# Optimization experiments

Measured on AMD Instinct MI355X. Metric: run time of the kernel, lower is better.

## Reference

```python
import jax, jax.numpy as jnp
import numpy as np

N, F_IN, F_OUT, HEADS = 4096, 128, 64, 4


def setup_inputs() -> dict:
    key = jax.random.key(0)
    k1, k2, k3, k4, k5 = jax.random.split(key, 5)
    X = jax.random.normal(k1, (N, F_IN), dtype=jnp.float32)
    A = jax.random.randint(k2, (N, N), 0, 2, dtype=jnp.int32)
    # zero the diagonal: the torch loop always prepends the self node, so the
    # adjacency must not also contain it (would duplicate the self term).
    A = A * (1 - jnp.eye(N, dtype=jnp.int32))
    # per-head Linear(F_IN, F_OUT) weights/bias and Linear(2*F_OUT, 1, bias=False)
    W = jax.random.normal(k3, (HEADS, F_OUT, F_IN), dtype=jnp.float32) / np.sqrt(F_IN)
    b = jax.random.normal(k4, (HEADS, F_OUT), dtype=jnp.float32) * 0.02
    att = jax.random.normal(k5, (HEADS, 2 * F_OUT), dtype=jnp.float32) / np.sqrt(2 * F_OUT)
    return {"X": X, "A": A, "W": W, "b": b, "att": att}


def reference(X, A, W, b, att):
    # H[h, n, o] = line_h(X)
    H = jnp.einsum('nf,hof->hno', X, W) + b[:, None, :]
    f_out = W.shape[1]
    a_src, a_dst = att[:, :f_out], att[:, f_out:]
    # score e_ij = leaky_relu(a_src.H_i + a_dst.H_j)
    s = jnp.einsum('hno,ho->hn', H, a_src)  # query-side term (xi_bar expanded)
    d = jnp.einsum('hno,ho->hn', H, a_dst)  # neighbor-side term
    e = jax.nn.leaky_relu(s[:, :, None] + d[:, None, :])  # [H, N, N]
    # neighbor set = {self} U {j : A_ij != 0}
    mask = (A > 0) | jnp.eye(A.shape[0], dtype=bool)
    e = jnp.where(mask[None], e, -jnp.inf)
    alpha = jax.nn.softmax(e, axis=-1)  # segment softmax per node row
    # weighted sum per head, then mean over heads (sum / head in the original)
    out = jnp.einsum('hnm,hmo->no', alpha, H) / W.shape[0]
    return out  # [N, F_OUT]
```

## Files before the change

### kernel.cpp

```cpp
#include <hip/hip_runtime.h>
#include <hip/hip_bf16.h>


#define NN 4096
#define FIN 128
#define FOUT 64
#define NH 4

typedef __attribute__((ext_vector_type(8))) short bf16x8;
typedef __attribute__((ext_vector_type(4))) float f32x4;
typedef __attribute__((ext_vector_type(4))) unsigned int u32x4;

__device__ __forceinline__ unsigned short f32_bf16(float f) {
    unsigned u = __builtin_bit_cast(unsigned, f);
    u += 0x7fffu + ((u >> 16) & 1u);
    return (unsigned short)(u >> 16);
}
__device__ __forceinline__ float bf16_f32(unsigned short h) {
    unsigned u = ((unsigned)h) << 16;
    return __builtin_bit_cast(float, u);
}

__global__ __launch_bounds__(256) void pack_bits(
    const int* __restrict__ A, unsigned long long* __restrict__ Abits)
{
    const int row  = blockIdx.x;
    const int lane = threadIdx.x & 63;
    const int wv   = threadIdx.x >> 6;
    const int* arow = A + (size_t)row * NN;
    #pragma unroll 4
    for (int c = 0; c < 16; ++c) {
        const int col = c * 256 + wv * 64 + lane;
        unsigned long long m = __ballot(arow[col] > 0);
        if (lane == 0) Abits[(size_t)row * 64 + c * 4 + wv] = m;
    }
}

__global__ __launch_bounds__(256) void gat_prep(
    const float* __restrict__ X, const float* __restrict__ W,
    const float* __restrict__ b, const float* __restrict__ att,
    unsigned short* __restrict__ HbfT,
    float* __restrict__ s_out, float* __restrict__ d_out,
    float* __restrict__ es_g, float* __restrict__ es2_g,
    float* __restrict__ ed_g, float* __restrict__ ed2_g)
{
    const int rb = blockIdx.x;
    const int h  = blockIdx.y;
    const int n0 = rb * 32;
    const int t  = threadIdx.x;

    __shared__ float Xl[32][132];
    __shared__ float Wt[128][68];

    for (int g = t; g < 32 * 32; g += 256) {
        int row = g >> 5, c4 = g & 31;
        float4 v = *(const float4*)&X[(size_t)(n0 + row) * FIN + c4 * 4];
        *(float4*)&Xl[row][c4 * 4] = v;
    }
    for (int g = t; g < 64 * 32; g += 256) {
        int o = g >> 5, c4 = g & 31;
        float4 v = *(const float4*)&W[((size_t)h * FOUT + o) * FIN + c4 * 4];
        Wt[c4 * 4 + 0][o] = v.x; Wt[c4 * 4 + 1][o] = v.y;
        Wt[c4 * 4 + 2][o] = v.z; Wt[c4 * 4 + 3][o] = v.w;
    }
    __syncthreads();

    const int rg = t >> 4;
    const int og = t & 15;
    float acc[2][4] = {};

    #pragma unroll 4
    for (int f4 = 0; f4 < 32; ++f4) {
        float xv[2][4], wv[4][4];
        #pragma unroll
        for (int i = 0; i < 2; ++i) {
            float4 tmp = *(const float4*)&Xl[rg * 2 + i][f4 * 4];
            xv[i][0] = tmp.x; xv[i][1] = tmp.y; xv[i][2] = tmp.z; xv[i][3] = tmp.w;
        }
        #pragma unroll
        for (int k = 0; k < 4; ++k) {
            float4 tmp = *(const float4*)&Wt[f4 * 4 + k][og * 4];
            wv[k][0] = tmp.x; wv[k][1] = tmp.y; wv[k][2] = tmp.z; wv[k][3] = tmp.w;
        }
        #pragma unroll
        for (int i = 0; i < 2; ++i)
            #pragma unroll
            for (int k = 0; k < 4; ++k)
                #pragma unroll
                for (int jj = 0; jj < 4; ++jj)
                    acc[i][jj] = fmaf(xv[i][k], wv[k][jj], acc[i][jj]);
    }

    float bb[4], as_[4], ad_[4];
    #pragma unroll
    for (int jj = 0; jj < 4; ++jj) {
        bb[jj]  = b[h * FOUT + og * 4 + jj];
        as_[jj] = att[h * 2 * FOUT + og * 4 + jj];
        ad_[jj] = att[h * 2 * FOUT + FOUT + og * 4 + jj];
    }
    #pragma unroll
    for (int i = 0; i < 2; ++i)
        #pragma unroll
        for (int jj = 0; jj < 4; ++jj)
            acc[i][jj] += bb[jj];

    float sp[2] = {0.f, 0.f}, dp[2] = {0.f, 0.f};
    #pragma unroll
    for (int i = 0; i < 2; ++i)
        #pragma unroll
        for (int jj = 0; jj < 4; ++jj) {
            sp[i] = fmaf(acc[i][jj], as_[jj], sp[i]);
            dp[i] = fmaf(acc[i][jj], ad_[jj], dp[i]);
        }
    #pragma unroll
    for (int off = 1; off < 16; off <<= 1) {
        #pragma unroll
        for (int i = 0; i < 2; ++i) {
            sp[i] += __shfl_xor(sp[i], off);
            dp[i] += __shfl_xor(dp[i], off);
        }
    }
    if (og == 0) {
        #pragma unroll
        for (int i = 0; i < 2; ++i) {
            int nn = n0 + rg * 2 + i;
            s_out[h * NN + nn]  = sp[i];
            d_out[h * NN + nn]  = dp[i];
            es_g [h * NN + nn]  = __expf(sp[i]);
            es2_g[h * NN + nn]  = __expf(0.01f * sp[i]);
            ed_g [h * NN + nn]  = __expf(dp[i]);
            ed2_g[h * NN + nn]  = __expf(0.01f * dp[i]);
        }
    }

    #pragma unroll
    for (int jj = 0; jj < 4; ++jj) {
        int o = og * 4 + jj;
        ushort2 p;
        p.x = f32_bf16(acc[0][jj]);
        p.y = f32_bf16(acc[1][jj]);
        *(ushort2*)&HbfT[((size_t)h * FOUT + o) * NN + n0 + rg * 2] = p;
    }
}

__global__ __launch_bounds__(512, 8) void gat_main(
    const unsigned* __restrict__ Abits, const unsigned short* __restrict__ HbfT,
    const float* __restrict__ es_g, const float* __restrict__ es2_g,
    const float* __restrict__ ed_g, const float* __restrict__ ed2_g,
    float* __restrict__ Hpart, float* __restrict__ lpartP)
{
    const int n0 = blockIdx.x * 128;
    const int cg = blockIdx.y;
    const int h  = blockIdx.z;
    const int tid  = threadIdx.x;
    const int w    = tid >> 6;
    const int lane = tid & 63;
    const int r    = lane & 15;
    const int q    = lane >> 4;

    __shared__ unsigned short Hlds[64][256];
    __shared__ unsigned bits_lds[128 * 9];

    const int n  = n0 + w * 16 + r;
    const float es  = es_g [h * NN + n];
    const float es2 = es2_g[h * NN + n];
    const int bits_base = (w * 16 + r) * 9;
    const int qs = q * 8;

    bf16x8 ones;
    #pragma unroll
    for (int i = 0; i < 8; ++i) ones[i] = (short)0x3F80;

    f32x4 acc0 = {0,0,0,0}, acc1 = {0,0,0,0}, acc2 = {0,0,0,0},
          acc3 = {0,0,0,0}, accl = {0,0,0,0};

    for (int ch = 0; ch < 4; ++ch) {
        const int c0 = cg * 1024 + ch * 256;
        __syncthreads();

        #pragma unroll
        for (int it = 0; it < 4; ++it) {
            int flat = it * 512 + tid;
            int o    = flat >> 5;
            int c16  = flat & 31;
            int blk  = c16 ^ (o & 31);
            *(bf16x8*)&Hlds[o][blk * 8] =
                *(const bf16x8*)&HbfT[((size_t)h * FOUT + o) * NN + c0 + c16 * 8];
        }
        #pragma unroll
        for (int it = 0; it < 2; ++it) {
            int flat = it * 512 + tid;
            int row = flat >> 3, wd = flat & 7;
            bits_lds[row * 9 + wd] = Abits[(size_t)(n0 + row) * 128 + (c0 >> 5) + wd];
        }
        __syncthreads();

        const float* edh  = ed_g  + h * NN + c0;
        const float* ed2h = ed2_g + h * NN + c0;

        #pragma unroll
        for (int step = 0; step < 8; ++step) {
            const unsigned bits8 = bits_lds[bits_base + step] >> qs;
            const int mk = step * 32 + qs;

            const float4 e0 = *(const float4*)&edh [mk];
            const float4 e1 = *(const float4*)&edh [mk + 4];
            const float4 g0 = *(const float4*)&ed2h[mk];
            const float4 g1 = *(const float4*)&ed2h[mk + 4];
            const float edv [8] = {e0.x, e0.y, e0.z, e0.w, e1.x, e1.y, e1.z, e1.w};
            const float ed2v[8] = {g0.x, g0.y, g0.z, g0.w, g1.x, g1.y, g1.z, g1.w};

            u32x4 afu;
            #pragma unroll
            for (int p = 0; p < 4; ++p) {
                const int j0 = 2 * p, j1 = 2 * p + 1;
                float wa = (bits8 & (1u << j0))
                         ? fmaxf(es * edv[j0], es2 * ed2v[j0]) : 0.0f;
                float wb = (bits8 & (1u << j1))
                         ? fmaxf(es * edv[j1], es2 * ed2v[j1]) : 0.0f;
                __hip_bfloat162 pk = __float22bfloat162_rn(make_float2(wa, wb));
                unsigned u;
                __builtin_memcpy(&u, &pk, sizeof(u));
                afu[p] = u;
            }
            const bf16x8 af = __builtin_bit_cast(bf16x8, afu);

            const int mb = step * 4 + q;
            const bf16x8 b0 = *(const bf16x8*)&Hlds[r     ][(mb ^ ((r     ) & 31)) * 8];
            const bf16x8 b1 = *(const bf16x8*)&Hlds[r + 16][(mb ^ ((r + 16) & 31)) * 8];
            const bf16x8 b2 = *(const bf16x8*)&Hlds[r + 32][(mb ^ ((r + 32) & 31)) * 8];
            const bf16x8 b3 = *(const bf16x8*)&Hlds[r + 48][(mb ^ ((r + 48) & 31)) * 8];

            acc0 = __builtin_amdgcn_mfma_f32_16x16x32_bf16(af, b0,   acc0, 0, 0, 0);
            acc1 = __builtin_amdgcn_mfma_f32_16x16x32_bf16(af, b1,   acc1, 0, 0, 0);
            acc2 = __builtin_amdgcn_mfma_f32_16x16x32_bf16(af, b2,   acc2, 0, 0, 0);
            acc3 = __builtin_amdgcn_mfma_f32_16x16x32_bf16(af, b3,   acc3, 0, 0, 0);
            accl = __builtin_amdgcn_mfma_f32_16x16x32_bf16(af, ones, accl, 0, 0, 0);
        }
    }

    float* hb = Hpart + ((size_t)(cg * NH + h) * NN + n0 + w * 16) * FOUT;
    #pragma unroll
    for (int reg = 0; reg < 4; ++reg) {
        const int rr = q * 4 + reg;
        hb[rr * FOUT +  0 + r] = acc0[reg];
        hb[rr * FOUT + 16 + r] = acc1[reg];
        hb[rr * FOUT + 32 + r] = acc2[reg];
        hb[rr * FOUT + 48 + r] = acc3[reg];
    }
    if (r == 0) {
        #pragma unroll
        for (int reg = 0; reg < 4; ++reg)
            lpartP[(size_t)(cg * NH + h) * NN + n0 + w * 16 + q * 4 + reg] = accl[reg];
    }
}

__global__ __launch_bounds__(256) void gat_fin(
    const float* __restrict__ Hpart, const unsigned short* __restrict__ HbfT,
    const float* __restrict__ lpartP, const float* __restrict__ s_g,
    const float* __restrict__ d_g, float* __restrict__ out)
{
    const int tid = threadIdx.x;
    const int rr  = tid >> 4;
    const int c4  = tid & 15;
    const int n   = blockIdx.x * 16 + rr;
    const int o   = c4 * 4;

    float4 res = make_float4(0.f, 0.f, 0.f, 0.f);
    #pragma unroll
    for (int h = 0; h < NH; ++h) {
        float l = 0.f;
        #pragma unroll
        for (int cg = 0; cg < 4; ++cg)
            l += lpartP[(size_t)(cg * NH + h) * NN + n];
        float tt = s_g[h * NN + n] + d_g[h * NN + n];
        float wd = __expf(fmaxf(tt, 0.01f * tt));
        float inv = 0.25f / (l + wd);

        float4 ha = make_float4(0.f, 0.f, 0.f, 0.f);
        #pragma unroll
        for (int cg = 0; cg < 4; ++cg) {
            float4 hp = *(const float4*)&Hpart[((size_t)(cg * NH + h) * NN + n) * FOUT + o];
            ha.x += hp.x; ha.y += hp.y; ha.z += hp.z; ha.w += hp.w;
        }
        float hd[4];
        #pragma unroll
        for (int jj = 0; jj < 4; ++jj)
            hd[jj] = bf16_f32(HbfT[((size_t)h * FOUT + o + jj) * NN + n]);

        res.x += (ha.x + wd * hd[0]) * inv;
        res.y += (ha.y + wd * hd[1]) * inv;
        res.z += (ha.z + wd * hd[2]) * inv;
        res.w += (ha.w + wd * hd[3]) * inv;
    }
    *(float4*)&out[(size_t)n * FOUT + o] = res;
}

extern "C" void kernel_launch(void* const* d_in, const int* in_sizes, int n_in,
                              void* d_out, int out_size, void* d_ws, size_t ws_size,
                              hipStream_t stream) {
    const float* X   = (const float*)d_in[0];
    const int*   A   = (const int*)  d_in[1];
    const float* W   = (const float*)d_in[2];
    const float* b   = (const float*)d_in[3];
    const float* att = (const float*)d_in[4];
    float* out = (float*)d_out;

    char* ws = (char*)d_ws;
    unsigned short* HbfT = (unsigned short*)ws;
    size_t off = (size_t)NH * FOUT * NN * 2;
    float* s_buf   = (float*)(ws + off);  off += (size_t)NH * NN * 4;
    float* d_buf   = (float*)(ws + off);  off += (size_t)NH * NN * 4;
    float* es_buf  = (float*)(ws + off);  off += (size_t)NH * NN * 4;
    float* es2_buf = (float*)(ws + off);  off += (size_t)NH * NN * 4;
    float* ed_buf  = (float*)(ws + off);  off += (size_t)NH * NN * 4;
    float* ed2_buf = (float*)(ws + off);  off += (size_t)NH * NN * 4;
    unsigned long long* Abits = (unsigned long long*)(ws + off);
    off += (size_t)NN * 64 * 8;
    float* Hpart  = (float*)(ws + off);
    off += (size_t)4 * NH * NN * FOUT * 4;
    float* lpartP = (float*)(ws + off);
    off += (size_t)4 * NH * NN * 4;

    pack_bits<<<NN, 256, 0, stream>>>(A, Abits);
    gat_prep<<<dim3(128, 4), 256, 0, stream>>>(X, W, b, att, HbfT, s_buf, d_buf,
                                               es_buf, es2_buf, ed_buf, ed2_buf);
    gat_main<<<dim3(32, 4, 4), 512, 0, stream>>>((const unsigned*)Abits, HbfT,
                                                 es_buf, es2_buf, ed_buf, ed2_buf,
                                                 Hpart, lpartP);
    gat_fin<<<256, 256, 0, stream>>>(Hpart, HbfT, lpartP, s_buf, d_buf, out);
}
```

Baseline: 188.5 us.

## Retile GAT main kernel to 64-row blocks with 2-way column split and streaming hints

```diff
diff --git a/kernel.cpp b/kernel.cpp
--- a/kernel.cpp
+++ b/kernel.cpp
@@ -15,10 +15,6 @@
     unsigned u = __builtin_bit_cast(unsigned, f);
     u += 0x7fffu + ((u >> 16) & 1u);
     return (unsigned short)(u >> 16);
-}
-__device__ __forceinline__ float bf16_f32(unsigned short h) {
-    unsigned u = ((unsigned)h) << 16;
-    return __builtin_bit_cast(float, u);
 }
 
 __global__ __launch_bounds__(256) void pack_bits(
@@ -31,7 +27,7 @@
     #pragma unroll 4
     for (int c = 0; c < 16; ++c) {
         const int col = c * 256 + wv * 64 + lane;
-        unsigned long long m = __ballot(arow[col] > 0);
+        unsigned long long m = __ballot(__builtin_nontemporal_load(&arow[col]) > 0);
         if (lane == 0) Abits[(size_t)row * 64 + c * 4 + wv] = m;
     }
 }
@@ -39,7 +35,7 @@
 __global__ __launch_bounds__(256) void gat_prep(
     const float* __restrict__ X, const float* __restrict__ W,
     const float* __restrict__ b, const float* __restrict__ att,
-    unsigned short* __restrict__ HbfT,
+    unsigned short* __restrict__ HbfT, float* __restrict__ Hrow,
     float* __restrict__ s_out, float* __restrict__ d_out,
     float* __restrict__ es_g, float* __restrict__ es2_g,
     float* __restrict__ ed_g, float* __restrict__ ed2_g)
@@ -134,6 +130,11 @@
     }
 
     #pragma unroll
+    for (int i = 0; i < 2; ++i) {
+        float4 v = make_float4(acc[i][0], acc[i][1], acc[i][2], acc[i][3]);
+        *(float4*)&Hrow[((size_t)h * NN + n0 + rg * 2 + i) * FOUT + og * 4] = v;
+    }
+    #pragma unroll
     for (int jj = 0; jj < 4; ++jj) {
         int o = og * 4 + jj;
         ushort2 p;
@@ -143,29 +144,32 @@
     }
 }
 
-__global__ __launch_bounds__(512, 8) void gat_main(
+__global__ __launch_bounds__(256, 8) void gat_main(
     const unsigned* __restrict__ Abits, const unsigned short* __restrict__ HbfT,
     const float* __restrict__ es_g, const float* __restrict__ es2_g,
     const float* __restrict__ ed_g, const float* __restrict__ ed2_g,
     float* __restrict__ Hpart, float* __restrict__ lpartP)
 {
-    const int n0 = blockIdx.x * 128;
-    const int cg = blockIdx.y;
-    const int h  = blockIdx.z;
+    const int id  = blockIdx.x;
+    const int grp = id & 7;
+    const int h   = grp >> 1;
+    const int cg  = grp & 1;
+    const int bx  = id >> 3;
+    const int n0  = bx * 64;
     const int tid  = threadIdx.x;
     const int w    = tid >> 6;
     const int lane = tid & 63;
     const int r    = lane & 15;
     const int q    = lane >> 4;
-
-    __shared__ unsigned short Hlds[64][256];
-    __shared__ unsigned bits_lds[128 * 9];
-
-    const int n  = n0 + w * 16 + r;
+    const int qs   = q * 8;
+
+    __shared__ unsigned short Hlds[64][128];
+    __shared__ unsigned bits_lds[64 * 5];
+
+    const int n = n0 + w * 16 + r;
     const float es  = es_g [h * NN + n];
     const float es2 = es2_g[h * NN + n];
-    const int bits_base = (w * 16 + r) * 9;
-    const int qs = q * 8;
+    const int bits_base = (w * 16 + r) * 5;
 
     bf16x8 ones;
     #pragma unroll
@@ -174,24 +178,22 @@
     f32x4 acc0 = {0,0,0,0}, acc1 = {0,0,0,0}, acc2 = {0,0,0,0},
           acc3 = {0,0,0,0}, accl = {0,0,0,0};
 
-    for (int ch = 0; ch < 4; ++ch) {
-        const int c0 = cg * 1024 + ch * 256;
+    for (int ch = 0; ch < 16; ++ch) {
+        const int c0 = cg * 2048 + ch * 128;
         __syncthreads();
 
         #pragma unroll
         for (int it = 0; it < 4; ++it) {
-            int flat = it * 512 + tid;
-            int o    = flat >> 5;
-            int c16  = flat & 31;
-            int blk  = c16 ^ (o & 31);
+            int flat = it * 256 + tid;
+            int o    = flat >> 4;
+            int c16  = flat & 15;
+            int blk  = c16 ^ (o & 15);
             *(bf16x8*)&Hlds[o][blk * 8] =
                 *(const bf16x8*)&HbfT[((size_t)h * FOUT + o) * NN + c0 + c16 * 8];
         }
-        #pragma unroll
-        for (int it = 0; it < 2; ++it) {
-            int flat = it * 512 + tid;
-            int row = flat >> 3, wd = flat & 7;
-            bits_lds[row * 9 + wd] = Abits[(size_t)(n0 + row) * 128 + (c0 >> 5) + wd];
+        {
+            int row = tid >> 2, wd = tid & 3;
+            bits_lds[row * 5 + wd] = Abits[(size_t)(n0 + row) * 128 + (c0 >> 5) + wd];
         }
         __syncthreads();
 
@@ -199,7 +201,7 @@
         const float* ed2h = ed2_g + h * NN + c0;
 
         #pragma unroll
-        for (int step = 0; step < 8; ++step) {
+        for (int step = 0; step < 4; ++step) {
             const unsigned bits8 = bits_lds[bits_base + step] >> qs;
             const int mk = step * 32 + qs;
 
@@ -225,11 +227,11 @@
             }
             const bf16x8 af = __builtin_bit_cast(bf16x8, afu);
 
-            const int mb = step * 4 + q;
-            const bf16x8 b0 = *(const bf16x8*)&Hlds[r     ][(mb ^ ((r     ) & 31)) * 8];
-            const bf16x8 b1 = *(const bf16x8*)&Hlds[r + 16][(mb ^ ((r + 16) & 31)) * 8];
-            const bf16x8 b2 = *(const bf16x8*)&Hlds[r + 32][(mb ^ ((r + 32) & 31)) * 8];
-            const bf16x8 b3 = *(const bf16x8*)&Hlds[r + 48][(mb ^ ((r + 48) & 31)) * 8];
+            const int mb = (step * 4 + q) ^ r;
+            const bf16x8 b0 = *(const bf16x8*)&Hlds[r     ][mb * 8];
+            const bf16x8 b1 = *(const bf16x8*)&Hlds[r + 16][mb * 8];
+            const bf16x8 b2 = *(const bf16x8*)&Hlds[r + 32][mb * 8];
+            const bf16x8 b3 = *(const bf16x8*)&Hlds[r + 48][mb * 8];
 
             acc0 = __builtin_amdgcn_mfma_f32_16x16x32_bf16(af, b0,   acc0, 0, 0, 0);
             acc1 = __builtin_amdgcn_mfma_f32_16x16x32_bf16(af, b1,   acc1, 0, 0, 0);
@@ -243,20 +245,21 @@
     #pragma unroll
     for (int reg = 0; reg < 4; ++reg) {
         const int rr = q * 4 + reg;
-        hb[rr * FOUT +  0 + r] = acc0[reg];
-        hb[rr * FOUT + 16 + r] = acc1[reg];
-        hb[rr * FOUT + 32 + r] = acc2[reg];
-        hb[rr * FOUT + 48 + r] = acc3[reg];
+        __builtin_nontemporal_store(acc0[reg], &hb[rr * FOUT +  0 + r]);
+        __builtin_nontemporal_store(acc1[reg], &hb[rr * FOUT + 16 + r]);
+        __builtin_nontemporal_store(acc2[reg], &hb[rr * FOUT + 32 + r]);
+        __builtin_nontemporal_store(acc3[reg], &hb[rr * FOUT + 48 + r]);
     }
     if (r == 0) {
         #pragma unroll
         for (int reg = 0; reg < 4; ++reg)
-            lpartP[(size_t)(cg * NH + h) * NN + n0 + w * 16 + q * 4 + reg] = accl[reg];
+            __builtin_nontemporal_store(accl[reg],
+                &lpartP[(size_t)(cg * NH + h) * NN + n0 + w * 16 + q * 4 + reg]);
     }
 }
 
 __global__ __launch_bounds__(256) void gat_fin(
-    const float* __restrict__ Hpart, const unsigned short* __restrict__ HbfT,
+    const float* __restrict__ Hpart, const float* __restrict__ Hrow,
     const float* __restrict__ lpartP, const float* __restrict__ s_g,
     const float* __restrict__ d_g, float* __restrict__ out)
 {
@@ -269,29 +272,22 @@
     float4 res = make_float4(0.f, 0.f, 0.f, 0.f);
     #pragma unroll
     for (int h = 0; h < NH; ++h) {
-        float l = 0.f;
-        #pragma unroll
-        for (int cg = 0; cg < 4; ++cg)
-            l += lpartP[(size_t)(cg * NH + h) * NN + n];
+        float l = lpartP[(size_t)h * NN + n]
+                + lpartP[(size_t)(NH + h) * NN + n];
         float tt = s_g[h * NN + n] + d_g[h * NN + n];
         float wd = __expf(fmaxf(tt, 0.01f * tt));
         float inv = 0.25f / (l + wd);
 
-        float4 ha = make_float4(0.f, 0.f, 0.f, 0.f);
-        #pragma unroll
-        for (int cg = 0; cg < 4; ++cg) {
-            float4 hp = *(const float4*)&Hpart[((size_t)(cg * NH + h) * NN + n) * FOUT + o];
-            ha.x += hp.x; ha.y += hp.y; ha.z += hp.z; ha.w += hp.w;
-        }
-        float hd[4];
-        #pragma unroll
-        for (int jj = 0; jj < 4; ++jj)
-            hd[jj] = bf16_f32(HbfT[((size_t)h * FOUT + o + jj) * NN + n]);
-
-        res.x += (ha.x + wd * hd[0]) * inv;
-        res.y += (ha.y + wd * hd[1]) * inv;
-        res.z += (ha.z + wd * hd[2]) * inv;
-        res.w += (ha.w + wd * hd[3]) * inv;
+        f32x4 h0 = __builtin_nontemporal_load(
+            (const f32x4*)&Hpart[((size_t)h * NN + n) * FOUT + o]);
+        f32x4 h1 = __builtin_nontemporal_load(
+            (const f32x4*)&Hpart[((size_t)(NH + h) * NN + n) * FOUT + o]);
+        float4 hr = *(const float4*)&Hrow[((size_t)h * NN + n) * FOUT + o];
+
+        res.x += (h0[0] + h1[0] + wd * hr.x) * inv;
+        res.y += (h0[1] + h1[1] + wd * hr.y) * inv;
+        res.z += (h0[2] + h1[2] + wd * hr.z) * inv;
+        res.w += (h0[3] + h1[3] + wd * hr.w) * inv;
     }
     *(float4*)&out[(size_t)n * FOUT + o] = res;
 }
@@ -317,16 +313,19 @@
     float* ed2_buf = (float*)(ws + off);  off += (size_t)NH * NN * 4;
     unsigned long long* Abits = (unsigned long long*)(ws + off);
     off += (size_t)NN * 64 * 8;
+    float* Hrow   = (float*)(ws + off);
+    off += (size_t)NH * NN * FOUT * 4;
     float* Hpart  = (float*)(ws + off);
-    off += (size_t)4 * NH * NN * FOUT * 4;
+    off += (size_t)2 * NH * NN * FOUT * 4;
     float* lpartP = (float*)(ws + off);
-    off += (size_t)4 * NH * NN * 4;
+    off += (size_t)2 * NH * NN * 4;
 
     pack_bits<<<NN, 256, 0, stream>>>(A, Abits);
-    gat_prep<<<dim3(128, 4), 256, 0, stream>>>(X, W, b, att, HbfT, s_buf, d_buf,
+    gat_prep<<<dim3(128, 4), 256, 0, stream>>>(X, W, b, att, HbfT, Hrow,
+                                               s_buf, d_buf,
                                                es_buf, es2_buf, ed_buf, ed2_buf);
-    gat_main<<<dim3(32, 4, 4), 512, 0, stream>>>((const unsigned*)Abits, HbfT,
-                                                 es_buf, es2_buf, ed_buf, ed2_buf,
-                                                 Hpart, lpartP);
-    gat_fin<<<256, 256, 0, stream>>>(Hpart, HbfT, lpartP, s_buf, d_buf, out);
-}
+    gat_main<<<512, 256, 0, stream>>>((const unsigned*)Abits, HbfT,
+                                      es_buf, es2_buf, ed_buf, ed2_buf,
+                                      Hpart, lpartP);
+    gat_fin<<<256, 256, 0, stream>>>(Hpart, Hrow, lpartP, s_buf, d_buf, out);
+}
```

After: 211.0 us. 11.9% more time.
